# Performance work log

Measured on AMD Instinct MI355X. Metric: run time of the kernel, lower is better.

Reference implementation:

```python
import jax, jax.numpy as jnp
import numpy as np

N, E = 50000, 800000
DN, DE, H, C = 64, 64, 4, 2
DH = DN // H


def setup_inputs() -> dict:
    key = jax.random.key(0)
    ks = jax.random.split(key, 12)
    def lin(k, fan_in, fan_out):
        return jax.random.normal(k, (fan_in, fan_out), dtype=jnp.float32) / np.sqrt(fan_in)
    return {
        "node_features": jax.random.normal(ks[0], (N, DN), dtype=jnp.float32),
        "edge_features": jax.random.normal(ks[1], (E, DE), dtype=jnp.float32),
        "edge_index": jax.random.randint(ks[2], (2, E), 0, N, dtype=jnp.int64),
        "Wq": lin(ks[3], DN, DN),
        "Wk": lin(ks[4], DN, DN),
        "Wv": lin(ks[5], DN, DN),
        "We": lin(ks[6], DE, DN),
        "Wo": lin(ks[7], DN, DN),
        "W1": lin(ks[8], 2 * DN + DE, DE),
        "b1": jnp.zeros((DE,), dtype=jnp.float32),
        "W2": lin(ks[9], DE, C),
        "b2": jnp.zeros((C,), dtype=jnp.float32),
    }


def reference(node_features, edge_features, edge_index, Wq, Wk, Wv, We, Wo, W1, b1, W2, b2):
    n = node_features.shape[0]
    src, tgt = edge_index[0], edge_index[1]

    # --- NodeAttention: multi-head attention over incoming edges ---
    q = (node_features @ Wq).reshape(n, H, DH)
    k = (node_features @ Wk).reshape(n, H, DH)
    v = (node_features @ Wv).reshape(n, H, DH)
    ep = (edge_features @ We).reshape(-1, H, DH)          # [E,H,DH]

    scores = jnp.sum(q[tgt] * (k[src] + ep), axis=-1) / np.sqrt(DH)  # [E,H]
    smax = jax.ops.segment_max(scores, tgt, num_segments=n)          # [N,H]
    ex = jnp.exp(scores - smax[tgt])
    denom = jax.ops.segment_sum(ex, tgt, num_segments=n)
    alpha = ex / (denom[tgt] + 1e-9)                                 # [E,H]

    msg = (alpha[..., None] * (v[src] + ep)).reshape(-1, H * DH)     # [E,DN]
    agg = jax.ops.segment_sum(msg, tgt, num_segments=n)              # [N,DN]
    new_nodes = node_features + agg @ Wo                             # residual

    # --- edge classifier: gather endpoints, concat edge feats, MLP+GELU ---
    edge_repr = jnp.concatenate([new_nodes[src], new_nodes[tgt], edge_features], axis=-1)
    h = jax.nn.gelu(edge_repr @ W1 + b1, approximate=False)
    return h @ W2 + b2
```

## Files before the change

### kernel.cpp

```cpp
#include <hip/hip_runtime.h>
#include <math.h>

typedef __attribute__((ext_vector_type(8))) short bf16x8;
typedef __attribute__((ext_vector_type(4))) float f32x4;

__device__ __forceinline__ short f2bf(float f) {
    unsigned u = __float_as_uint(f);
    unsigned r = (u + 0x7FFFu + ((u >> 16) & 1u)) >> 16;
    return (short)r;
}

__device__ __forceinline__ int swz(int row, int kbyte) {
    return kbyte ^ ((row & 7) << 4);
}

__global__ __launch_bounds__(256) void hist_kernel(
    const int* __restrict__ eidx, int* __restrict__ cnt, int E)
{
    for (long e = (long)blockIdx.x * blockDim.x + threadIdx.x; e < E;
         e += (long)gridDim.x * blockDim.x)
        atomicAdd(&cnt[eidx[E + e]], 1);
}

__global__ __launch_bounds__(1024) void scan_kernel(
    const int* __restrict__ cnt, int* __restrict__ cursor, int N)
{
    __shared__ int pa[1024], pb[1024];
    int t = threadIdx.x;
    int chunk = (N + 1023) >> 10;
    int lo = t * chunk, hi = min(lo + chunk, N);
    int s = 0;
    for (int j = lo; j < hi; j++) s += cnt[j];
    pa[t] = s;
    __syncthreads();
    int* src = pa; int* dst = pb;
    for (int off = 1; off < 1024; off <<= 1) {
        int val = src[t];
        if (t >= off) val += src[t - off];
        dst[t] = val;
        __syncthreads();
        int* tmp = src; src = dst; dst = tmp;
    }
    int excl = (t == 0) ? 0 : src[t - 1];
    for (int j = lo; j < hi; j++) { cursor[j] = excl; excl += cnt[j]; }
}

__global__ __launch_bounds__(256) void scatter_kernel(
    const int* __restrict__ eidx, int* __restrict__ cursor,
    int* __restrict__ sorted, int E)
{
    for (long e = (long)blockIdx.x * blockDim.x + threadIdx.x; e < E;
         e += (long)gridDim.x * blockDim.x) {
        int tg = eidx[E + e];
        int pos = atomicAdd(&cursor[tg], 1);
        sorted[pos] = (int)e;
    }
}

__global__ __launch_bounds__(256) void qkv_kernel(
    const float* __restrict__ x,
    const float* __restrict__ Wq, const float* __restrict__ Wk, const float* __restrict__ Wv,
    float* __restrict__ q, float* __restrict__ k, float* __restrict__ v, int N)
{
    __shared__ float sW[3][64][64];
    __shared__ float sx[4][64];
    int t = threadIdx.x;
    for (int i = t; i < 4096; i += 256) {
        sW[0][i >> 6][i & 63] = Wq[i];
        sW[1][i >> 6][i & 63] = Wk[i];
        sW[2][i >> 6][i & 63] = Wv[i];
    }
    __syncthreads();
    int c = t & 63, sub = t >> 6;
    for (int base = blockIdx.x * 4; base < N; base += gridDim.x * 4) {
        int n = base + sub;
        if (n < N) sx[sub][c] = x[(size_t)n * 64 + c];
        __syncthreads();
        if (n < N) {
            float aq = 0.f, ak = 0.f, av = 0.f;
            #pragma unroll
            for (int i = 0; i < 64; i++) {
                float xv = sx[sub][i];
                aq += xv * sW[0][i][c];
                ak += xv * sW[1][i][c];
                av += xv * sW[2][i][c];
            }
            q[(size_t)n * 64 + c] = aq;
            k[(size_t)n * 64 + c] = ak;
            v[(size_t)n * 64 + c] = av;
        }
        __syncthreads();
    }
}

__device__ __forceinline__ void stage_w64T(const float* __restrict__ W, short* sWT, int t) {
    for (int i = t; i < 4096; i += 256) {
        int k = i >> 6, n = i & 63;
        short vv = f2bf(W[i]);
        int kb = k * 2;
        int off = n * 128 + (swz(n, kb & ~15) | (kb & 15));
        *(short*)((char*)sWT + off) = vv;
    }
}

__global__ __launch_bounds__(256) void edge_kernel(
    const float* __restrict__ ef, const int* __restrict__ eidx,
    const int* __restrict__ sorted,
    const float* __restrict__ q, const float* __restrict__ k,
    const float* __restrict__ v, const float* __restrict__ We,
    float* __restrict__ denom, float* __restrict__ agg, int E)
{
    __shared__ short sWeT[4096];
    __shared__ float ep_lds[64 * 66];
    __shared__ float ex_lds[64 * 4];
    __shared__ int sedge[64], sidx[64], tidx[64];
    int t = threadIdx.x;
    stage_w64T(We, sWeT, t);
    __syncthreads();

    int lane = t & 63, w = t >> 6;
    int ntiles = E >> 6;
    for (int tile = blockIdx.x; tile < ntiles; tile += gridDim.x) {
        size_t tile64 = (size_t)tile * 64;
        if (t < 64) {
            int se = sorted[tile64 + t];
            sedge[t] = se;
            sidx[t] = eidx[se];
            tidx[t] = eidx[E + se];
        }
        __syncthreads();

        {
            f32x4 acc[4];
            #pragma unroll
            for (int nt = 0; nt < 4; nt++) acc[nt] = (f32x4){0.f, 0.f, 0.f, 0.f};
            int erow = sedge[w * 16 + (lane & 15)];
            #pragma unroll
            for (int kk = 0; kk < 2; kk++) {
                const float* base = ef + (size_t)erow * 64 + kk * 32 + (lane >> 4) * 8;
                float4 x0 = *(const float4*)(base);
                float4 x1 = *(const float4*)(base + 4);
                bf16x8 a;
                a[0] = f2bf(x0.x); a[1] = f2bf(x0.y); a[2] = f2bf(x0.z); a[3] = f2bf(x0.w);
                a[4] = f2bf(x1.x); a[5] = f2bf(x1.y); a[6] = f2bf(x1.z); a[7] = f2bf(x1.w);
                #pragma unroll
                for (int nt = 0; nt < 4; nt++) {
                    int n = nt * 16 + (lane & 15);
                    int kb = kk * 64 + (lane >> 4) * 16;
                    bf16x8 b = *(const bf16x8*)((const char*)sWeT + n * 128 + swz(n, kb));
                    acc[nt] = __builtin_amdgcn_mfma_f32_16x16x32_bf16(a, b, acc[nt], 0, 0, 0);
                }
            }
            #pragma unroll
            for (int nt = 0; nt < 4; nt++)
                #pragma unroll
                for (int r = 0; r < 4; r++) {
                    int row = w * 16 + (lane >> 4) * 4 + r;
                    int col = nt * 16 + (lane & 15);
                    ep_lds[row * 66 + col] = acc[nt][r];
                }
        }
        __syncthreads();

        {
            int e_loc = t >> 2, h = t & 3;
            int src = sidx[e_loc], tgt = tidx[e_loc];
            const float4* qp = (const float4*)(q + (size_t)tgt * 64 + h * 16);
            const float4* kp = (const float4*)(k + (size_t)src * 64 + h * 16);
            const float* epp = ep_lds + e_loc * 66 + h * 16;
            float s = 0.f;
            #pragma unroll
            for (int j = 0; j < 4; j++) {
                float4 qq = qp[j];
                float4 kk = kp[j];
                s += qq.x * (kk.x + epp[j * 4 + 0]);
                s += qq.y * (kk.y + epp[j * 4 + 1]);
                s += qq.z * (kk.z + epp[j * 4 + 2]);
                s += qq.w * (kk.w + epp[j * 4 + 3]);
            }
            ex_lds[e_loc * 4 + h] = __expf(s * 0.25f);
        }
        __syncthreads();

        {
            int h = lane >> 4;
            float vv[16];
            #pragma unroll
            for (int i = 0; i < 16; i++)
                vv[i] = v[(size_t)sidx[w * 16 + i] * 64 + lane];
            int cur = tidx[w * 16];
            float acc = 0.f, den = 0.f;
            #pragma unroll
            for (int i = 0; i < 16; i++) {
                int e_loc = w * 16 + i;
                int tg = tidx[e_loc];
                if (tg != cur) {
                    atomicAdd(&agg[(size_t)cur * 64 + lane], acc);
                    if ((lane & 15) == 0) atomicAdd(&denom[(size_t)cur * 4 + h], den);
                    acc = 0.f; den = 0.f; cur = tg;
                }
                float ex = ex_lds[e_loc * 4 + h];
                acc += ex * (vv[i] + ep_lds[e_loc * 66 + lane]);
                den += ex;
            }
            atomicAdd(&agg[(size_t)cur * 64 + lane], acc);
            if ((lane & 15) == 0) atomicAdd(&denom[(size_t)cur * 4 + h], den);
        }
        __syncthreads();
    }
}

__global__ __launch_bounds__(256) void wo_kernel(
    const float* __restrict__ agg, const float* __restrict__ denom,
    const float* __restrict__ x,
    const float* __restrict__ Wo, short* __restrict__ out_bf, int N)
{
    __shared__ float sW[64][64];
    __shared__ float sx[4][64];
    int t = threadIdx.x;
    for (int i = t; i < 4096; i += 256) sW[i >> 6][i & 63] = Wo[i];
    __syncthreads();
    int c = t & 63, sub = t >> 6;
    for (int base = blockIdx.x * 4; base < N; base += gridDim.x * 4) {
        int n = base + sub;
        if (n < N) {
            float d = denom[(size_t)n * 4 + (c >> 4)] + 1e-9f;
            sx[sub][c] = agg[(size_t)n * 64 + c] / d;
        }
        __syncthreads();
        if (n < N) {
            float acc = 0.f;
            #pragma unroll
            for (int i = 0; i < 64; i++) acc += sx[sub][i] * sW[i][c];
            out_bf[(size_t)n * 64 + c] = f2bf(x[(size_t)n * 64 + c] + acc);
        }
        __syncthreads();
    }
}

__global__ __launch_bounds__(256, 4) void cls_kernel(
    const short* __restrict__ nnb, const float* __restrict__ ef,
    const int* __restrict__ eidx,
    const float* __restrict__ W1, const float* __restrict__ b1,
    const float* __restrict__ W2, const float* __restrict__ b2,
    float* __restrict__ out, int E)
{
    __shared__ short sWt1[64 * 192];
    __shared__ float sW2[128];
    __shared__ float sb1[64];
    __shared__ float sb2[2];
    __shared__ int sidx[64], tidx[64];
    int t = threadIdx.x;
    for (int i = t; i < 192 * 64; i += 256) {
        int k = i >> 6, n = i & 63;
        short vv = f2bf(W1[i]);
        int kb = k * 2;
        int off = n * 384 + (swz(n, kb & ~15) | (kb & 15));
        *(short*)((char*)sWt1 + off) = vv;
    }
    if (t < 128) sW2[t] = W2[t];
    if (t < 64) sb1[t] = b1[t];
    if (t < 2) sb2[t] = b2[t];
    __syncthreads();

    int lane = t & 63, w = t >> 6;
    int ntiles = E >> 6;
    for (int tile = blockIdx.x; tile < ntiles; tile += gridDim.x) {
        size_t tile64 = (size_t)tile * 64;
        if (t < 64) {
            sidx[t] = eidx[tile64 + t];
            tidx[t] = eidx[(size_t)E + tile64 + t];
        }
        __syncthreads();

        f32x4 acc[4];
        #pragma unroll
        for (int nt = 0; nt < 4; nt++) acc[nt] = (f32x4){0.f, 0.f, 0.f, 0.f};

        int e16 = w * 16 + (lane & 15);
        #pragma unroll
        for (int kk = 0; kk < 6; kk++) {
            bf16x8 a;
            if (kk < 4) {
                int nd = (kk < 2) ? sidx[e16] : tidx[e16];
                a = *(const bf16x8*)(nnb + (size_t)nd * 64 + (kk & 1) * 32 + (lane >> 4) * 8);
            } else {
                const float* base = ef + (tile64 + (size_t)e16) * 64 + (kk - 4) * 32;
                const float4* p = (const float4*)(base + (lane >> 4) * 8);
                float4 x0 = p[0], x1 = p[1];
                a[0] = f2bf(x0.x); a[1] = f2bf(x0.y); a[2] = f2bf(x0.z); a[3] = f2bf(x0.w);
                a[4] = f2bf(x1.x); a[5] = f2bf(x1.y); a[6] = f2bf(x1.z); a[7] = f2bf(x1.w);
            }
            #pragma unroll
            for (int nt = 0; nt < 4; nt++) {
                int n = nt * 16 + (lane & 15);
                int kb = kk * 64 + (lane >> 4) * 16;
                bf16x8 b = *(const bf16x8*)((const char*)sWt1 + n * 384 + swz(n, kb));
                acc[nt] = __builtin_amdgcn_mfma_f32_16x16x32_bf16(a, b, acc[nt], 0, 0, 0);
            }
        }

        #pragma unroll
        for (int r = 0; r < 4; r++) {
            float p0 = 0.f, p1 = 0.f;
            #pragma unroll
            for (int nt = 0; nt < 4; nt++) {
                int col = nt * 16 + (lane & 15);
                float h = acc[nt][r] + sb1[col];
                float g = 0.5f * h * (1.f + erff(h * 0.70710678118654752f));
                p0 += g * sW2[col * 2 + 0];
                p1 += g * sW2[col * 2 + 1];
            }
            #pragma unroll
            for (int o = 1; o < 16; o <<= 1) {
                p0 += __shfl_xor(p0, o, 64);
                p1 += __shfl_xor(p1, o, 64);
            }
            if ((lane & 15) == 0) {
                int row = w * 16 + (lane >> 4) * 4 + r;
                out[(tile64 + (size_t)row) * 2 + 0] = p0 + sb2[0];
                out[(tile64 + (size_t)row) * 2 + 1] = p1 + sb2[1];
            }
        }
        __syncthreads();
    }
}

extern "C" void kernel_launch(void* const* d_in, const int* in_sizes, int n_in,
                              void* d_out, int out_size, void* d_ws, size_t ws_size,
                              hipStream_t stream)
{
    const float* node = (const float*)d_in[0];
    const float* ef   = (const float*)d_in[1];
    const int*   eidx = (const int*)d_in[2];
    const float* Wq   = (const float*)d_in[3];
    const float* Wk   = (const float*)d_in[4];
    const float* Wv   = (const float*)d_in[5];
    const float* We   = (const float*)d_in[6];
    const float* Wo   = (const float*)d_in[7];
    const float* W1   = (const float*)d_in[8];
    const float* b1   = (const float*)d_in[9];
    const float* W2   = (const float*)d_in[10];
    const float* b2   = (const float*)d_in[11];
    float* out = (float*)d_out;

    int N = in_sizes[0] / 64;
    int E = in_sizes[1] / 64;
    size_t N64 = (size_t)N * 64;

    float* q      = (float*)d_ws;
    float* k      = q + N64;
    float* v      = k + N64;
    float* agg    = v + N64;
    float* denom  = agg + N64;
    int*   cnt    = (int*)(denom + (size_t)N * 4);
    int*   cursor = cnt + N;
    int*   sorted = cursor + N;
    short* newnb  = (short*)(sorted + E);

    hipMemsetAsync(agg, 0, (N64 + (size_t)N * 4 + (size_t)N) * 4, stream);

    hist_kernel<<<2048, 256, 0, stream>>>(eidx, cnt, E);
    scan_kernel<<<1, 1024, 0, stream>>>(cnt, cursor, N);
    scatter_kernel<<<2048, 256, 0, stream>>>(eidx, cursor, sorted, E);
    qkv_kernel<<<512, 256, 0, stream>>>(node, Wq, Wk, Wv, q, k, v, N);
    edge_kernel<<<2048, 256, 0, stream>>>(ef, eidx, sorted, q, k, v, We, denom, agg, E);
    wo_kernel<<<512, 256, 0, stream>>>(agg, denom, node, Wo, newnb, N);
    cls_kernel<<<2048, 256, 0, stream>>>(newnb, ef, eidx, W1, b1, W2, b2, out, E);
}
```

Before: 693.0 us.

## Use MFMA for node projections, bf16 q/k/v, parallel scan, packed sorted edges

The single-block serial scan is replaced with a three-kernel multi-block scan. The scatter now writes packed (edge, src, tgt) records so the edge kernel avoids dependent index gathers. The qkv and Wo projections move from scalar FP32 loops to bf16 MFMA tiles, and q/k/v are stored as bf16 to halve gather traffic in the edge kernel. Edge-feature streaming loads become nontemporal. Together these target the serial scan bottleneck and the memory-bound gathers, at the cost of reduced precision in q/k/v and the aggregation input, plus extra launches.

New measurement: 560.2 us. -19.2%, faster.

```diff
diff --git a/kernel.cpp b/kernel.cpp
--- a/kernel.cpp
+++ b/kernel.cpp
@@ -9,6 +9,9 @@
     unsigned r = (u + 0x7FFFu + ((u >> 16) & 1u)) >> 16;
     return (short)r;
 }
+__device__ __forceinline__ float bf2f(short s) {
+    return __uint_as_float(((unsigned)(unsigned short)s) << 16);
+}
 
 __device__ __forceinline__ int swz(int row, int kbyte) {
     return kbyte ^ ((row & 7) << 4);
@@ -22,92 +25,137 @@
         atomicAdd(&cnt[eidx[E + e]], 1);
 }
 
-__global__ __launch_bounds__(1024) void scan_kernel(
-    const int* __restrict__ cnt, int* __restrict__ cursor, int N)
-{
-    __shared__ int pa[1024], pb[1024];
-    int t = threadIdx.x;
-    int chunk = (N + 1023) >> 10;
-    int lo = t * chunk, hi = min(lo + chunk, N);
-    int s = 0;
-    for (int j = lo; j < hi; j++) s += cnt[j];
-    pa[t] = s;
-    __syncthreads();
-    int* src = pa; int* dst = pb;
-    for (int off = 1; off < 1024; off <<= 1) {
-        int val = src[t];
-        if (t >= off) val += src[t - off];
-        dst[t] = val;
-        __syncthreads();
-        int* tmp = src; src = dst; dst = tmp;
-    }
-    int excl = (t == 0) ? 0 : src[t - 1];
-    for (int j = lo; j < hi; j++) { cursor[j] = excl; excl += cnt[j]; }
+__global__ __launch_bounds__(256) void scanA_kernel(
+    const int* __restrict__ cnt, int* __restrict__ tmp, int* __restrict__ bsum, int N)
+{
+    __shared__ int sa[256], sb_[256];
+    int t = threadIdx.x;
+    int i = blockIdx.x * 256 + t;
+    int val = (i < N) ? cnt[i] : 0;
+    sa[t] = val;
+    __syncthreads();
+    int* src = sa; int* dst = sb_;
+    for (int off = 1; off < 256; off <<= 1) {
+        int v2 = src[t];
+        if (t >= off) v2 += src[t - off];
+        dst[t] = v2;
+        __syncthreads();
+        int* tm = src; src = dst; dst = tm;
+    }
+    if (i < N) tmp[i] = src[t];
+    if (t == 255) bsum[blockIdx.x] = src[255];
+}
+
+__global__ __launch_bounds__(256) void scanB_kernel(
+    const int* __restrict__ bsum, int* __restrict__ boff, int NB)
+{
+    __shared__ int sa[256], sb_[256];
+    int t = threadIdx.x;
+    int val = (t < NB) ? bsum[t] : 0;
+    sa[t] = val;
+    __syncthreads();
+    int* src = sa; int* dst = sb_;
+    for (int off = 1; off < 256; off <<= 1) {
+        int v2 = src[t];
+        if (t >= off) v2 += src[t - off];
+        dst[t] = v2;
+        __syncthreads();
+        int* tm = src; src = dst; dst = tm;
+    }
+    if (t < NB) boff[t] = src[t] - val;
+}
+
+__global__ __launch_bounds__(256) void scanC_kernel(
+    const int* __restrict__ cnt, const int* __restrict__ tmp,
+    const int* __restrict__ boff, int* __restrict__ cursor, int N)
+{
+    int i = blockIdx.x * 256 + threadIdx.x;
+    if (i < N) cursor[i] = tmp[i] - cnt[i] + boff[blockIdx.x];
 }
 
 __global__ __launch_bounds__(256) void scatter_kernel(
     const int* __restrict__ eidx, int* __restrict__ cursor,
-    int* __restrict__ sorted, int E)
+    int4* __restrict__ sortedq, int E)
 {
     for (long e = (long)blockIdx.x * blockDim.x + threadIdx.x; e < E;
          e += (long)gridDim.x * blockDim.x) {
+        int sr = eidx[e];
         int tg = eidx[E + e];
         int pos = atomicAdd(&cursor[tg], 1);
-        sorted[pos] = (int)e;
+        sortedq[pos] = make_int4((int)e, sr, tg, 0);
     }
 }
 
 __global__ __launch_bounds__(256) void qkv_kernel(
     const float* __restrict__ x,
     const float* __restrict__ Wq, const float* __restrict__ Wk, const float* __restrict__ Wv,
-    float* __restrict__ q, float* __restrict__ k, float* __restrict__ v, int N)
-{
-    __shared__ float sW[3][64][64];
-    __shared__ float sx[4][64];
+    short* __restrict__ qb, short* __restrict__ kb_, short* __restrict__ vb, int N)
+{
+    __shared__ short sWT[12288];
     int t = threadIdx.x;
     for (int i = t; i < 4096; i += 256) {
-        sW[0][i >> 6][i & 63] = Wq[i];
-        sW[1][i >> 6][i & 63] = Wk[i];
-        sW[2][i >> 6][i & 63] = Wv[i];
-    }
-    __syncthreads();
-    int c = t & 63, sub = t >> 6;
-    for (int base = blockIdx.x * 4; base < N; base += gridDim.x * 4) {
-        int n = base + sub;
-        if (n < N) sx[sub][c] = x[(size_t)n * 64 + c];
-        __syncthreads();
-        if (n < N) {
-            float aq = 0.f, ak = 0.f, av = 0.f;
-            #pragma unroll
-            for (int i = 0; i < 64; i++) {
-                float xv = sx[sub][i];
-                aq += xv * sW[0][i][c];
-                ak += xv * sW[1][i][c];
-                av += xv * sW[2][i][c];
-            }
-            q[(size_t)n * 64 + c] = aq;
-            k[(size_t)n * 64 + c] = ak;
-            v[(size_t)n * 64 + c] = av;
-        }
-        __syncthreads();
-    }
+        int k = i >> 6, n = i & 63;
+        int kby = k * 2;
+        int off = n * 128 + (swz(n, kby & ~15) | (kby & 15));
+        *(short*)((char*)sWT + off) = f2bf(Wq[i]);
+        *(short*)((char*)sWT + 8192 + off) = f2bf(Wk[i]);
+        *(short*)((char*)sWT + 16384 + off) = f2bf(Wv[i]);
+    }
+    __syncthreads();
+
+    int lane = t & 63, w = t >> 6;
+    int tile = blockIdx.x;
+    f32x4 acc[12];
+    #pragma unroll
+    for (int nt = 0; nt < 12; nt++) acc[nt] = (f32x4){0.f, 0.f, 0.f, 0.f};
+
+    int gr = tile * 64 + w * 16 + (lane & 15);
+    int grc = min(gr, N - 1);
+    #pragma unroll
+    for (int kk = 0; kk < 2; kk++) {
+        const float* base = x + (size_t)grc * 64 + kk * 32 + (lane >> 4) * 8;
+        float4 x0 = *(const float4*)(base);
+        float4 x1 = *(const float4*)(base + 4);
+        bf16x8 a;
+        a[0] = f2bf(x0.x); a[1] = f2bf(x0.y); a[2] = f2bf(x0.z); a[3] = f2bf(x0.w);
+        a[4] = f2bf(x1.x); a[5] = f2bf(x1.y); a[6] = f2bf(x1.z); a[7] = f2bf(x1.w);
+        #pragma unroll
+        for (int nt = 0; nt < 12; nt++) {
+            int ng = nt * 16 + (lane & 15);
+            int kby = kk * 64 + (lane >> 4) * 16;
+            bf16x8 b = *(const bf16x8*)((const char*)sWT + ng * 128 + swz(ng, kby));
+            acc[nt] = __builtin_amdgcn_mfma_f32_16x16x32_bf16(a, b, acc[nt], 0, 0, 0);
+        }
+    }
+    #pragma unroll
+    for (int nt = 0; nt < 12; nt++)
+        #pragma unroll
+        for (int r = 0; r < 4; r++) {
+            int row = tile * 64 + w * 16 + (lane >> 4) * 4 + r;
+            if (row < N) {
+                int col = nt * 16 + (lane & 15);
+                short vv = f2bf(acc[nt][r]);
+                if (col < 64)       qb[(size_t)row * 64 + col] = vv;
+                else if (col < 128) kb_[(size_t)row * 64 + col - 64] = vv;
+                else                vb[(size_t)row * 64 + col - 128] = vv;
+            }
+        }
 }
 
 __device__ __forceinline__ void stage_w64T(const float* __restrict__ W, short* sWT, int t) {
     for (int i = t; i < 4096; i += 256) {
         int k = i >> 6, n = i & 63;
         short vv = f2bf(W[i]);
-        int kb = k * 2;
-        int off = n * 128 + (swz(n, kb & ~15) | (kb & 15));
+        int kby = k * 2;
+        int off = n * 128 + (swz(n, kby & ~15) | (kby & 15));
         *(short*)((char*)sWT + off) = vv;
     }
 }
 
 __global__ __launch_bounds__(256) void edge_kernel(
-    const float* __restrict__ ef, const int* __restrict__ eidx,
-    const int* __restrict__ sorted,
-    const float* __restrict__ q, const float* __restrict__ k,
-    const float* __restrict__ v, const float* __restrict__ We,
+    const float* __restrict__ ef, const int4* __restrict__ sortedq,
+    const short* __restrict__ qb, const short* __restrict__ kb_,
+    const short* __restrict__ vb, const float* __restrict__ We,
     float* __restrict__ denom, float* __restrict__ agg, int E)
 {
     __shared__ short sWeT[4096];
@@ -123,10 +171,10 @@
     for (int tile = blockIdx.x; tile < ntiles; tile += gridDim.x) {
         size_t tile64 = (size_t)tile * 64;
         if (t < 64) {
-            int se = sorted[tile64 + t];
-            sedge[t] = se;
-            sidx[t] = eidx[se];
-            tidx[t] = eidx[E + se];
+            int4 rec = sortedq[tile64 + t];
+            sedge[t] = rec.x;
+            sidx[t] = rec.y;
+            tidx[t] = rec.z;
         }
         __syncthreads();
 
@@ -137,17 +185,17 @@
             int erow = sedge[w * 16 + (lane & 15)];
             #pragma unroll
             for (int kk = 0; kk < 2; kk++) {
-                const float* base = ef + (size_t)erow * 64 + kk * 32 + (lane >> 4) * 8;
-                float4 x0 = *(const float4*)(base);
-                float4 x1 = *(const float4*)(base + 4);
+                const f32x4* base = (const f32x4*)(ef + (size_t)erow * 64 + kk * 32 + (lane >> 4) * 8);
+                f32x4 x0 = __builtin_nontemporal_load(base);
+                f32x4 x1 = __builtin_nontemporal_load(base + 1);
                 bf16x8 a;
                 a[0] = f2bf(x0.x); a[1] = f2bf(x0.y); a[2] = f2bf(x0.z); a[3] = f2bf(x0.w);
                 a[4] = f2bf(x1.x); a[5] = f2bf(x1.y); a[6] = f2bf(x1.z); a[7] = f2bf(x1.w);
                 #pragma unroll
                 for (int nt = 0; nt < 4; nt++) {
                     int n = nt * 16 + (lane & 15);
-                    int kb = kk * 64 + (lane >> 4) * 16;
-                    bf16x8 b = *(const bf16x8*)((const char*)sWeT + n * 128 + swz(n, kb));
+                    int kby = kk * 64 + (lane >> 4) * 16;
+                    bf16x8 b = *(const bf16x8*)((const char*)sWeT + n * 128 + swz(n, kby));
                     acc[nt] = __builtin_amdgcn_mfma_f32_16x16x32_bf16(a, b, acc[nt], 0, 0, 0);
                 }
             }
@@ -165,19 +213,16 @@
         {
             int e_loc = t >> 2, h = t & 3;
             int src = sidx[e_loc], tgt = tidx[e_loc];
-            const float4* qp = (const float4*)(q + (size_t)tgt * 64 + h * 16);
-            const float4* kp = (const float4*)(k + (size_t)src * 64 + h * 16);
+            const bf16x8* qp = (const bf16x8*)(qb + (size_t)tgt * 64 + h * 16);
+            const bf16x8* kp = (const bf16x8*)(kb_ + (size_t)src * 64 + h * 16);
+            bf16x8 q0 = qp[0], q1 = qp[1];
+            bf16x8 k0 = kp[0], k1 = kp[1];
             const float* epp = ep_lds + e_loc * 66 + h * 16;
             float s = 0.f;
             #pragma unroll
-            for (int j = 0; j < 4; j++) {
-                float4 qq = qp[j];
-                float4 kk = kp[j];
-                s += qq.x * (kk.x + epp[j * 4 + 0]);
-                s += qq.y * (kk.y + epp[j * 4 + 1]);
-                s += qq.z * (kk.z + epp[j * 4 + 2]);
-                s += qq.w * (kk.w + epp[j * 4 + 3]);
-            }
+            for (int j = 0; j < 8; j++) s += bf2f(q0[j]) * (bf2f(k0[j]) + epp[j]);
+            #pragma unroll
+            for (int j = 0; j < 8; j++) s += bf2f(q1[j]) * (bf2f(k1[j]) + epp[8 + j]);
             ex_lds[e_loc * 4 + h] = __expf(s * 0.25f);
         }
         __syncthreads();
@@ -187,7 +232,7 @@
             float vv[16];
             #pragma unroll
             for (int i = 0; i < 16; i++)
-                vv[i] = v[(size_t)sidx[w * 16 + i] * 64 + lane];
+                vv[i] = bf2f(vb[(size_t)sidx[w * 16 + i] * 64 + lane]);
             int cur = tidx[w * 16];
             float acc = 0.f, den = 0.f;
             #pragma unroll
@@ -213,29 +258,53 @@
 __global__ __launch_bounds__(256) void wo_kernel(
     const float* __restrict__ agg, const float* __restrict__ denom,
     const float* __restrict__ x,
-    const float* __restrict__ Wo, short* __restrict__ out_bf, int N)
-{
-    __shared__ float sW[64][64];
-    __shared__ float sx[4][64];
-    int t = threadIdx.x;
-    for (int i = t; i < 4096; i += 256) sW[i >> 6][i & 63] = Wo[i];
-    __syncthreads();
-    int c = t & 63, sub = t >> 6;
-    for (int base = blockIdx.x * 4; base < N; base += gridDim.x * 4) {
-        int n = base + sub;
-        if (n < N) {
-            float d = denom[(size_t)n * 4 + (c >> 4)] + 1e-9f;
-            sx[sub][c] = agg[(size_t)n * 64 + c] / d;
-        }
-        __syncthreads();
-        if (n < N) {
-            float acc = 0.f;
-            #pragma unroll
-            for (int i = 0; i < 64; i++) acc += sx[sub][i] * sW[i][c];
-            out_bf[(size_t)n * 64 + c] = f2bf(x[(size_t)n * 64 + c] + acc);
-        }
-        __syncthreads();
-    }
+    const float* __restrict__ Wo, short* __restrict__ nnb, int N)
+{
+    __shared__ short sWT[4096];
+    int t = threadIdx.x;
+    stage_w64T(Wo, sWT, t);
+    __syncthreads();
+
+    int lane = t & 63, w = t >> 6;
+    int tile = blockIdx.x;
+    f32x4 acc[4];
+    #pragma unroll
+    for (int nt = 0; nt < 4; nt++) acc[nt] = (f32x4){0.f, 0.f, 0.f, 0.f};
+
+    int gr = tile * 64 + w * 16 + (lane & 15);
+    int grc = min(gr, N - 1);
+    #pragma unroll
+    for (int kk = 0; kk < 2; kk++) {
+        int fbase = kk * 32 + (lane >> 4) * 8;
+        int h = fbase >> 4;
+        float d = denom[(size_t)grc * 4 + h] + 1e-9f;
+        const float* base = agg + (size_t)grc * 64 + fbase;
+        float4 x0 = *(const float4*)(base);
+        float4 x1 = *(const float4*)(base + 4);
+        float inv = 1.f / d;
+        bf16x8 a;
+        a[0] = f2bf(x0.x * inv); a[1] = f2bf(x0.y * inv);
+        a[2] = f2bf(x0.z * inv); a[3] = f2bf(x0.w * inv);
+        a[4] = f2bf(x1.x * inv); a[5] = f2bf(x1.y * inv);
+        a[6] = f2bf(x1.z * inv); a[7] = f2bf(x1.w * inv);
+        #pragma unroll
+        for (int nt = 0; nt < 4; nt++) {
+            int n = nt * 16 + (lane & 15);
+            int kby = kk * 64 + (lane >> 4) * 16;
+            bf16x8 b = *(const bf16x8*)((const char*)sWT + n * 128 + swz(n, kby));
+            acc[nt] = __builtin_amdgcn_mfma_f32_16x16x32_bf16(a, b, acc[nt], 0, 0, 0);
+        }
+    }
+    #pragma unroll
+    for (int nt = 0; nt < 4; nt++)
+        #pragma unroll
+        for (int r = 0; r < 4; r++) {
+            int row = tile * 64 + w * 16 + (lane >> 4) * 4 + r;
+            if (row < N) {
+                int col = nt * 16 + (lane & 15);
+                nnb[(size_t)row * 64 + col] = f2bf(x[(size_t)row * 64 + col] + acc[nt][r]);
+            }
+        }
 }
 
 __global__ __launch_bounds__(256, 4) void cls_kernel(
@@ -254,8 +323,8 @@
     for (int i = t; i < 192 * 64; i += 256) {
         int k = i >> 6, n = i & 63;
         short vv = f2bf(W1[i]);
-        int kb = k * 2;
-        int off = n * 384 + (swz(n, kb & ~15) | (kb & 15));
+        int kby = k * 2;
+        int off = n * 384 + (swz(n, kby & ~15) | (kby & 15));
         *(short*)((char*)sWt1 + off) = vv;
     }
     if (t < 128) sW2[t] = W2[t];
@@ -285,17 +354,18 @@
                 int nd = (kk < 2) ? sidx[e16] : tidx[e16];
                 a = *(const bf16x8*)(nnb + (size_t)nd * 64 + (kk & 1) * 32 + (lane >> 4) * 8);
             } else {
-                const float* base = ef + (tile64 + (size_t)e16) * 64 + (kk - 4) * 32;
-                const float4* p = (const float4*)(base + (lane >> 4) * 8);
-                float4 x0 = p[0], x1 = p[1];
+                const f32x4* p = (const f32x4*)(ef + (tile64 + (size_t)e16) * 64
+                                                + (kk - 4) * 32 + (lane >> 4) * 8);
+                f32x4 x0 = __builtin_nontemporal_load(p);
+                f32x4 x1 = __builtin_nontemporal_load(p + 1);
                 a[0] = f2bf(x0.x); a[1] = f2bf(x0.y); a[2] = f2bf(x0.z); a[3] = f2bf(x0.w);
                 a[4] = f2bf(x1.x); a[5] = f2bf(x1.y); a[6] = f2bf(x1.z); a[7] = f2bf(x1.w);
             }
             #pragma unroll
             for (int nt = 0; nt < 4; nt++) {
                 int n = nt * 16 + (lane & 15);
-                int kb = kk * 64 + (lane >> 4) * 16;
-                bf16x8 b = *(const bf16x8*)((const char*)sWt1 + n * 384 + swz(n, kb));
+                int kby = kk * 64 + (lane >> 4) * 16;
+                bf16x8 b = *(const bf16x8*)((const char*)sWt1 + n * 384 + swz(n, kby));
                 acc[nt] = __builtin_amdgcn_mfma_f32_16x16x32_bf16(a, b, acc[nt], 0, 0, 0);
             }
         }
@@ -347,24 +417,30 @@
     int N = in_sizes[0] / 64;
     int E = in_sizes[1] / 64;
     size_t N64 = (size_t)N * 64;
-
-    float* q      = (float*)d_ws;
-    float* k      = q + N64;
-    float* v      = k + N64;
-    float* agg    = v + N64;
-    float* denom  = agg + N64;
-    int*   cnt    = (int*)(denom + (size_t)N * 4);
+    int NB = (N + 255) / 256;
+
+    int4*  sortedq = (int4*)d_ws;
+    short* qb   = (short*)(sortedq + E);
+    short* kb_  = qb + N64;
+    short* vb   = kb_ + N64;
+    short* nnb  = vb + N64;
+    float* agg  = (float*)(nnb + N64);
+    float* denom = agg + N64;
+    int*   cnt   = (int*)(denom + (size_t)N * 4);
     int*   cursor = cnt + N;
-    int*   sorted = cursor + N;
-    short* newnb  = (short*)(sorted + E);
+    int*   tmp    = cursor + N;
+    int*   bsum   = tmp + N;
+    int*   boff   = bsum + 256;
 
     hipMemsetAsync(agg, 0, (N64 + (size_t)N * 4 + (size_t)N) * 4, stream);
 
     hist_kernel<<<2048, 256, 0, stream>>>(eidx, cnt, E);
-    scan_kernel<<<1, 1024, 0, stream>>>(cnt, cursor, N);
-    scatter_kernel<<<2048, 256, 0, stream>>>(eidx, cursor, sorted, E);
-    qkv_kernel<<<512, 256, 0, stream>>>(node, Wq, Wk, Wv, q, k, v, N);
-    edge_kernel<<<2048, 256, 0, stream>>>(ef, eidx, sorted, q, k, v, We, denom, agg, E);
-    wo_kernel<<<512, 256, 0, stream>>>(agg, denom, node, Wo, newnb, N);
-    cls_kernel<<<2048, 256, 0, stream>>>(newnb, ef, eidx, W1, b1, W2, b2, out, E);
-}
+    scanA_kernel<<<NB, 256, 0, stream>>>(cnt, tmp, bsum, N);
+    scanB_kernel<<<1, 256, 0, stream>>>(bsum, boff, NB);
+    scanC_kernel<<<NB, 256, 0, stream>>>(cnt, tmp, boff, cursor, N);
+    scatter_kernel<<<2048, 256, 0, stream>>>(eidx, cursor, sortedq, E);
+    qkv_kernel<<<(N + 63) / 64, 256, 0, stream>>>(node, Wq, Wk, Wv, qb, kb_, vb, N);
+    edge_kernel<<<2048, 256, 0, stream>>>(ef, sortedq, qb, kb_, vb, We, denom, agg, E);
+    wo_kernel<<<(N + 63) / 64, 256, 0, stream>>>(agg, denom, node, Wo, nnb, N);
+    cls_kernel<<<2048, 256, 0, stream>>>(nnb, ef, eidx, W1, b1, W2, b2, out, E);
+}
```
